# Kernel optimization log

Measured on AMD Instinct MI355X. Metric: run time of the kernel, lower is better.

Reference implementation:

```python
import jax, jax.numpy as jnp
import numpy as np

EMBED_DIM, NUM_HEADS, LOCAL_SIZE = 256, 4, 15
HEAD_DIM = EMBED_DIM // NUM_HEADS
SCALING = float(HEAD_DIM) ** -0.5


def get_overlap_segments(x, window_size):
    # x: (n, t, d) -> (n, t, window_size, d), zero-padded local windows centered at each position
    n, t, d = x.shape
    p = (window_size - 1) // 2
    xp = jnp.pad(x, ((0, 0), (p, p), (0, 0)))
    idx = jnp.arange(t)[:, None] + jnp.arange(window_size)[None, :]  # (t, w)
    return xp[:, idx]


def setup_inputs():
    key = jax.random.key(0)
    ks = jax.random.split(key, 4)
    B, W, F = 4, 64, 4096
    T = W + F
    x = jax.random.normal(ks[0], (B, T, EMBED_DIM), dtype=jnp.float32)
    # block one-hot frame->window assignment (each window owns F//W consecutive frames)
    assign = jnp.repeat(jnp.arange(W), F // W)
    wm = jnp.broadcast_to(jax.nn.one_hot(assign, W, dtype=jnp.float32).T[None], (B, W, F))
    W_qkv = jax.random.normal(ks[1], (EMBED_DIM, 3 * EMBED_DIM), jnp.float32) * 0.02
    b_qkv = jnp.zeros((3 * EMBED_DIM,), jnp.float32)
    W_out = jax.random.normal(ks[2], (EMBED_DIM, EMBED_DIM), jnp.float32) * 0.02
    b_out = jnp.zeros((EMBED_DIM,), jnp.float32)
    return {"x": x, "window_mapping": wm, "W_qkv": W_qkv, "b_qkv": b_qkv,
            "W_out": W_out, "b_out": b_out}


def _to_heads(z, b, t):
    # (b, t, E) -> (b*H, t, d), matching torch transpose/reshape ordering (b outer, h inner)
    return z.reshape(b, t, NUM_HEADS, HEAD_DIM).transpose(0, 2, 1, 3).reshape(b * NUM_HEADS, t, HEAD_DIM)


def reference(x, window_mapping, W_qkv, b_qkv, W_out, b_out):
    b, t, e = x.shape
    Wn, Fn = window_mapping.shape[1], window_mapping.shape[2]
    qkv = x @ W_qkv + b_qkv
    Q, K, V = jnp.split(qkv, 3, axis=-1)
    Q = Q * SCALING
    wtok = _to_heads(x[:, :Wn], b, Wn)            # (n, W, d) raw word tokens
    Qh = _to_heads(Q, b, t)[:, Wn:]               # (n, F, d)
    Kh = _to_heads(K, b, t)[:, Wn:]
    Vh = _to_heads(V, b, t)[:, Wn:]
    wm = jnp.broadcast_to(window_mapping[:, None], (b, NUM_HEADS, Wn, Fn)).reshape(b * NUM_HEADS, Wn, Fn)
    # scatter each window's word token to its frames
    expa = jnp.einsum('nwd,nwf->nfd', wtok, wm)   # (n, F, d)
    Kseg = get_overlap_segments(Kh, LOCAL_SIZE)   # (n, F, w, d)
    Vseg = get_overlap_segments(Vh, LOCAL_SIZE)
    Kcat = jnp.concatenate([expa[:, :, None], Kseg], axis=2)  # (n, F, 1+w, d)
    scores = jnp.einsum('nfd,nfwd->nfw', Qh, Kcat)            # (n, F, 1+w)
    # word-token weight: softmax across frames within each window chunk (F % W == 0, no pad)
    chunk = Fn // Wn
    w_wtok = jax.nn.softmax(scores[:, :, 0].reshape(-1, Wn, chunk), axis=-1).reshape(-1, Fn)
    # local-window weights: softmax over the window axis
    w_fea = jax.nn.softmax(scores[:, :, 1:], axis=-1)
    attn = jnp.concatenate([w_wtok[:, :, None], w_fea], axis=2)  # (n, F, 1+w)
    Vcat = jnp.concatenate([expa[:, :, None], Vseg], axis=2)
    out_fea = jnp.einsum('nfw,nfwd->nfd', attn, Vcat)            # (n, F, d)
    out = jnp.concatenate([wtok, out_fea], axis=1)               # (n, T, d)
    out = out.reshape(b, NUM_HEADS, t, HEAD_DIM).transpose(0, 2, 1, 3).reshape(b, t, e)
    return out @ W_out + b_out
```

## Files before the change

### kernel.cpp

```cpp
#include <hip/hip_runtime.h>


#define QN 4194304ull

typedef _Float16 h8 __attribute__((ext_vector_type(8)));
typedef _Float16 h4 __attribute__((ext_vector_type(4)));
typedef _Float16 h2 __attribute__((ext_vector_type(2)));
typedef float f32x16 __attribute__((ext_vector_type(16)));

__global__ __launch_bounds__(256) void conv_small(
    const float* __restrict__ x,
    const float* __restrict__ Wq, const float* __restrict__ Wo,
    _Float16* __restrict__ wqth, _Float16* __restrict__ woth,
    _Float16* __restrict__ xh) {
  const int g = blockIdx.x, tid = threadIdx.x;
  if (g < 768) {
    int o = g * 256 + tid;
    int n = o >> 8, k = o & 255;
    wqth[o] = (_Float16)Wq[(size_t)k * 768 + n];
  } else if (g < 1024) {
    int o = (g - 768) * 256 + tid;
    int n = o >> 8, k = o & 255;
    woth[o] = (_Float16)Wo[(size_t)k * 256 + n];
  } else {
    size_t base = (size_t)(g - 1024) * 4096 + (size_t)tid * 4;
#pragma unroll
    for (int c = 0; c < 4; ++c) {
      float4 v = *(const float4*)(x + base + c * 1024);
      h4 hv = {(_Float16)v.x, (_Float16)v.y, (_Float16)v.z, (_Float16)v.w};
      *(h4*)(xh + base + c * 1024) = hv;
    }
  }
}

__global__ __launch_bounds__(256) void qkv_mfma(
    const _Float16* __restrict__ xh, const _Float16* __restrict__ wth,
    const float* __restrict__ bq,
    _Float16* __restrict__ Qh, _Float16* __restrict__ Kh,
    _Float16* __restrict__ Vh) {
  __shared__ _Float16 Ah[128][40], Bh[128][40];
  const int tid = threadIdx.x;
  const int wave = tid >> 6, lane = tid & 63;
  const int ln = lane & 31, half = lane >> 5;
  const int mw = (wave & 1) * 64, nw = (wave >> 1) * 64;
  const int m0 = blockIdx.x * 128, n0 = blockIdx.y * 128;

  const int sr = tid >> 1, scq = (tid & 1) * 16;
  const int am = m0 + sr;
  const size_t arow =
      ((size_t)((am >> 12) * 4160 + 64 + (am & 4095))) * 256 + scq;
  const size_t brow = (size_t)(n0 + sr) * 256 + scq;

  float4 rah0, rah1, rbh0, rbh1;
  auto QLOAD = [&](int k0_) {
    rah0 = *(const float4*)(xh + arow + k0_);
    rah1 = *(const float4*)(xh + arow + k0_ + 8);
    rbh0 = *(const float4*)(wth + brow + k0_);
    rbh1 = *(const float4*)(wth + brow + k0_ + 8);
  };

  QLOAD(0);
  f32x16 acc[2][2] = {};

  for (int it = 0; it < 8; ++it) {
    __syncthreads();
    *(float4*)&Ah[sr][scq] = rah0;
    *(float4*)&Ah[sr][scq + 8] = rah1;
    *(float4*)&Bh[sr][scq] = rbh0;
    *(float4*)&Bh[sr][scq + 8] = rbh1;
    __syncthreads();
    if (it < 7) QLOAD((it + 1) * 32);
#pragma unroll
    for (int ks = 0; ks < 2; ++ks) {
      const int kc = ks * 16 + half * 8;
      h8 a0 = *(const h8*)&Ah[mw + ln][kc];
      h8 a1 = *(const h8*)&Ah[mw + 32 + ln][kc];
      h8 b0 = *(const h8*)&Bh[nw + ln][kc];
      h8 b1 = *(const h8*)&Bh[nw + 32 + ln][kc];
      acc[0][0] = __builtin_amdgcn_mfma_f32_32x32x16_f16(a0, b0, acc[0][0], 0, 0, 0);
      acc[0][1] = __builtin_amdgcn_mfma_f32_32x32x16_f16(a0, b1, acc[0][1], 0, 0, 0);
      acc[1][0] = __builtin_amdgcn_mfma_f32_32x32x16_f16(a1, b0, acc[1][0], 0, 0, 0);
      acc[1][1] = __builtin_amdgcn_mfma_f32_32x32x16_f16(a1, b1, acc[1][1], 0, 0, 0);
    }
  }

#pragma unroll
  for (int ni = 0; ni < 2; ++ni) {
    const int c = n0 + nw + ni * 32 + ln;
    const int which = c >> 8, e = c & 255;
    const int h = e >> 6, d = e & 63;
    _Float16* dst = (which == 0) ? Qh : (which == 1) ? Kh : Vh;
    const float sc2 = (which == 0) ? 0.125f : 1.0f;
    const float bias = bq[c];
#pragma unroll
    for (int mi = 0; mi < 2; ++mi) {
      const int rb = m0 + mw + mi * 32 + 4 * half;
#pragma unroll
      for (int reg = 0; reg < 16; ++reg) {
        int rr = rb + (reg & 3) + 8 * (reg >> 2);
        int b2 = rr >> 12, f2 = rr & 4095;
        dst[(((size_t)(b2 * 4 + h)) * 4096 + f2) * 64 + d] =
            (_Float16)((acc[mi][ni][reg] + bias) * sc2);
      }
    }
  }
}

__global__ __launch_bounds__(256) void attn_fused(
    const _Float16* __restrict__ Qh, const _Float16* __restrict__ Kh,
    const _Float16* __restrict__ Vh, const _Float16* __restrict__ xh,
    _Float16* __restrict__ OFh) {
  __shared__ _Float16 Ks[78][72];
  __shared__ _Float16 Vs[78][72];
  __shared__ float s0s[64];
  __shared__ float red[2];
  const int tid = threadIdx.x;
  const int w = blockIdx.x;
  const int n = blockIdx.y;
  const int f0 = w * 64;
  const int b = n >> 2, h = n & 3;

  for (int idx = tid; idx < 78 * 8; idx += 256) {
    int rr = idx >> 3, c = (idx & 7) * 8;
    int g = f0 - 7 + rr;
    h8 k8 = {}, v8 = {};
    if (g >= 0 && g < 4096) {
      size_t base = ((size_t)n * 4096 + g) * 64 + c;
      k8 = *(const h8*)(Kh + base);
      v8 = *(const h8*)(Vh + base);
    }
    *(h8*)&Ks[rr][c] = k8;
    *(h8*)&Vs[rr][c] = v8;
  }
  __syncthreads();

  const int i = tid >> 2, q = tid & 3;
  const size_t qbase = ((size_t)n * 4096 + f0 + i) * 64 + q * 16;
  h8 qh0 = *(const h8*)(Qh + qbase);
  h8 qh1 = *(const h8*)(Qh + qbase + 8);
  const size_t wbase = ((size_t)(b * 4160 + w)) * 256 + h * 64 + q * 16;
  h8 e0 = *(const h8*)(xh + wbase);
  h8 e1 = *(const h8*)(xh + wbase + 8);

  auto dot8 = [](h8 a, h8 bb, float s) {
    s = __builtin_amdgcn_fdot2((h2){a.s0, a.s1}, (h2){bb.s0, bb.s1}, s, false);
    s = __builtin_amdgcn_fdot2((h2){a.s2, a.s3}, (h2){bb.s2, bb.s3}, s, false);
    s = __builtin_amdgcn_fdot2((h2){a.s4, a.s5}, (h2){bb.s4, bb.s5}, s, false);
    s = __builtin_amdgcn_fdot2((h2){a.s6, a.s7}, (h2){bb.s6, bb.s7}, s, false);
    return s;
  };

  float s0 = dot8(qh1, e1, dot8(qh0, e0, 0.f));
  s0 += __shfl_xor(s0, 1);
  s0 += __shfl_xor(s0, 2);

  float sj[15];
#pragma unroll
  for (int j = 0; j < 15; ++j) {
    h8 k0 = *(const h8*)&Ks[i + j][q * 16];
    h8 k1 = *(const h8*)&Ks[i + j][q * 16 + 8];
    float s = dot8(qh1, k1, dot8(qh0, k0, 0.f));
    s += __shfl_xor(s, 1);
    s += __shfl_xor(s, 2);
    sj[j] = s;
  }

  if (q == 0) s0s[i] = s0;
  __syncthreads();
  if (tid < 64) {
    float v = s0s[tid];
    float m = v;
    for (int o = 1; o < 64; o <<= 1) m = fmaxf(m, __shfl_xor(m, o));
    float ee = __expf(v - m);
    float s = ee;
    for (int o = 1; o < 64; o <<= 1) s += __shfl_xor(s, o);
    if (tid == 0) { red[0] = m; red[1] = s; }
  }
  __syncthreads();
  const float wt = __expf(s0 - red[0]) / red[1];

  float mx = sj[0];
#pragma unroll
  for (int j = 1; j < 15; ++j) mx = fmaxf(mx, sj[j]);
  float pj[15], den = 0.f;
#pragma unroll
  for (int j = 0; j < 15; ++j) { pj[j] = __expf(sj[j] - mx); den += pj[j]; }
  const float inv = 1.0f / den;

  float o[16];
#pragma unroll
  for (int k = 0; k < 8; ++k) o[k] = wt * (float)e0[k];
#pragma unroll
  for (int k = 0; k < 8; ++k) o[8 + k] = wt * (float)e1[k];
#pragma unroll
  for (int j = 0; j < 15; ++j) {
    float wj = pj[j] * inv;
    h8 v0 = *(const h8*)&Vs[i + j][q * 16];
    h8 v1 = *(const h8*)&Vs[i + j][q * 16 + 8];
    o[0] = fmaf(wj, (float)v0.s0, o[0]);
    o[1] = fmaf(wj, (float)v0.s1, o[1]);
    o[2] = fmaf(wj, (float)v0.s2, o[2]);
    o[3] = fmaf(wj, (float)v0.s3, o[3]);
    o[4] = fmaf(wj, (float)v0.s4, o[4]);
    o[5] = fmaf(wj, (float)v0.s5, o[5]);
    o[6] = fmaf(wj, (float)v0.s6, o[6]);
    o[7] = fmaf(wj, (float)v0.s7, o[7]);
    o[8] = fmaf(wj, (float)v1.s0, o[8]);
    o[9] = fmaf(wj, (float)v1.s1, o[9]);
    o[10] = fmaf(wj, (float)v1.s2, o[10]);
    o[11] = fmaf(wj, (float)v1.s3, o[11]);
    o[12] = fmaf(wj, (float)v1.s4, o[12]);
    o[13] = fmaf(wj, (float)v1.s5, o[13]);
    o[14] = fmaf(wj, (float)v1.s6, o[14]);
    o[15] = fmaf(wj, (float)v1.s7, o[15]);
  }
  _Float16 oh[16];
#pragma unroll
  for (int dd = 0; dd < 16; ++dd) oh[dd] = (_Float16)o[dd];
  *(float4*)(OFh + qbase) = *(float4*)&oh[0];
  *(float4*)(OFh + qbase + 8) = *(float4*)&oh[8];
}

__global__ __launch_bounds__(256) void out_mfma(
    const _Float16* __restrict__ xh, const _Float16* __restrict__ ofh,
    const _Float16* __restrict__ wth, const float* __restrict__ bo,
    float* __restrict__ out) {
  __shared__ _Float16 Ah[64][72], Bh[128][72];
  const int tid = threadIdx.x;
  const int wave = tid >> 6, lane = tid & 63;
  const int ln = lane & 31, half = lane >> 5;
  const int mw = (wave & 1) * 32, nw = (wave >> 1) * 64;
  const int m0 = blockIdx.x * 64, n0 = blockIdx.y * 128;

  const int sr = tid >> 2, sc4 = (tid & 3) * 16;
  const int sr2 = tid >> 1, sc2 = (tid & 1) * 32;

  const int m = m0 + sr;
  const int b = m / 4160, tt = m % 4160;
  const bool useX = (tt < 64);
  const size_t xrow = ((size_t)(b * 4160 + tt)) * 256 + sc4;
  const long obase = ((long)(b * 4) * 4096 + (tt - 64)) * 64 + sc4;
  const size_t bbase = (size_t)(n0 + sr2) * 256 + sc2;

  float4 ra0, ra1, rb0, rb1, rb2, rb3;
  auto OLOAD = [&](int k0_) {
    if (useX) {
      ra0 = *(const float4*)(xh + xrow + k0_);
      ra1 = *(const float4*)(xh + xrow + k0_ + 8);
    } else {
      size_t o_ = (size_t)(obase + (long)(k0_ >> 6) * 262144);
      ra0 = *(const float4*)(ofh + o_);
      ra1 = *(const float4*)(ofh + o_ + 8);
    }
    rb0 = *(const float4*)(wth + bbase + k0_);
    rb1 = *(const float4*)(wth + bbase + k0_ + 8);
    rb2 = *(const float4*)(wth + bbase + k0_ + 16);
    rb3 = *(const float4*)(wth + bbase + k0_ + 24);
  };

  OLOAD(0);
  f32x16 acc0 = {}, acc1 = {};
  for (int it = 0; it < 4; ++it) {
    __syncthreads();
    *(float4*)&Ah[sr][sc4] = ra0;
    *(float4*)&Ah[sr][sc4 + 8] = ra1;
    *(float4*)&Bh[sr2][sc2] = rb0;
    *(float4*)&Bh[sr2][sc2 + 8] = rb1;
    *(float4*)&Bh[sr2][sc2 + 16] = rb2;
    *(float4*)&Bh[sr2][sc2 + 24] = rb3;
    __syncthreads();
    if (it < 3) OLOAD((it + 1) * 64);
#pragma unroll
    for (int ks = 0; ks < 4; ++ks) {
      const int kc = ks * 16 + half * 8;
      h8 ah = *(const h8*)&Ah[mw + ln][kc];
      h8 b0 = *(const h8*)&Bh[nw + ln][kc];
      h8 b1 = *(const h8*)&Bh[nw + 32 + ln][kc];
      acc0 = __builtin_amdgcn_mfma_f32_32x32x16_f16(ah, b0, acc0, 0, 0, 0);
      acc1 = __builtin_amdgcn_mfma_f32_32x32x16_f16(ah, b1, acc1, 0, 0, 0);
    }
  }
  const int rb = m0 + mw + 4 * half;
#pragma unroll
  for (int ni = 0; ni < 2; ++ni) {
    const int c = n0 + nw + ni * 32 + ln;
    const float bias = bo[c];
    const f32x16& a = ni ? acc1 : acc0;
#pragma unroll
    for (int reg = 0; reg < 16; ++reg) {
      int rr = rb + (reg & 3) + 8 * (reg >> 2);
      out[(size_t)rr * 256 + c] = a[reg] + bias;
    }
  }
}

extern "C" void kernel_launch(void* const* d_in, const int* in_sizes, int n_in,
                              void* d_out, int out_size, void* d_ws, size_t ws_size,
                              hipStream_t stream) {
  const float* x  = (const float*)d_in[0];
  const float* Wq = (const float*)d_in[2];
  const float* bq = (const float*)d_in[3];
  const float* Wo = (const float*)d_in[4];
  const float* bo = (const float*)d_in[5];
  float* out = (float*)d_out;

  _Float16* Qh   = (_Float16*)d_ws;
  _Float16* Kh   = Qh + QN;
  _Float16* Vh   = Kh + QN;
  _Float16* OFh  = Vh + QN;
  _Float16* Wqth = OFh + QN;
  _Float16* Woth = Wqth + 196608;
  _Float16* xh   = Woth + 65536;

  conv_small<<<dim3(2064), 256, 0, stream>>>(x, Wq, Wo, Wqth, Woth, xh);
  qkv_mfma<<<dim3(128, 6), 256, 0, stream>>>(xh, Wqth, bq, Qh, Kh, Vh);
  attn_fused<<<dim3(64, 16), 256, 0, stream>>>(Qh, Kh, Vh, xh, OFh);
  out_mfma<<<dim3(260, 2), 256, 0, stream>>>(xh, OFh, Woth, bo, out);
}
```

Measured before the change: 115.4 us.

## Fuse x fp16 conversion into QKV GEMM and shrink pre-conversion kernel

The QKV GEMM now reads fp32 x directly and converts to fp16 in registers, so the full-x conversion pass is gone. Only the 64 word-token rows per batch are still converted to fp16 (needed later by attention and the output GEMM), along with the W_out transpose. Both are done by an extra row of blocks in the GEMM grid. The W_qkv transpose moves to a small kernel that uses LDS tiling for coalesced reads and writes. The trade-off is that the GEMM reads twice the bytes for its A operand.

```diff
diff --git a/kernel.cpp b/kernel.cpp
--- a/kernel.cpp
+++ b/kernel.cpp
@@ -8,38 +8,77 @@
 typedef _Float16 h2 __attribute__((ext_vector_type(2)));
 typedef float f32x16 __attribute__((ext_vector_type(16)));
 
-__global__ __launch_bounds__(256) void conv_small(
-    const float* __restrict__ x,
-    const float* __restrict__ Wq, const float* __restrict__ Wo,
-    _Float16* __restrict__ wqth, _Float16* __restrict__ woth,
-    _Float16* __restrict__ xh) {
-  const int g = blockIdx.x, tid = threadIdx.x;
-  if (g < 768) {
-    int o = g * 256 + tid;
-    int n = o >> 8, k = o & 255;
-    wqth[o] = (_Float16)Wq[(size_t)k * 768 + n];
-  } else if (g < 1024) {
-    int o = (g - 768) * 256 + tid;
-    int n = o >> 8, k = o & 255;
-    woth[o] = (_Float16)Wo[(size_t)k * 256 + n];
-  } else {
-    size_t base = (size_t)(g - 1024) * 4096 + (size_t)tid * 4;
-#pragma unroll
-    for (int c = 0; c < 4; ++c) {
-      float4 v = *(const float4*)(x + base + c * 1024);
-      h4 hv = {(_Float16)v.x, (_Float16)v.y, (_Float16)v.z, (_Float16)v.w};
-      *(h4*)(xh + base + c * 1024) = hv;
-    }
+__global__ __launch_bounds__(256) void wq_t(
+    const float* __restrict__ Wq, _Float16* __restrict__ wqth) {
+  __shared__ float S[64 * 65];
+  const int id = blockIdx.x, tid = threadIdx.x;
+  const int k0 = (id & 3) * 64, n0 = (id >> 2) * 64;
+  {
+    const int r = tid >> 2, c0 = (tid & 3) * 16;
+    const float* src = Wq + (size_t)(k0 + r) * 768 + n0 + c0;
+#pragma unroll
+    for (int cc = 0; cc < 16; cc += 4)
+      *(float4*)&S[r * 65 + c0 + cc] = *(const float4*)(src + cc);
+  }
+  __syncthreads();
+  {
+    const int nl = tid >> 2, kl0 = (tid & 3) * 16;
+    _Float16 hh[16];
+#pragma unroll
+    for (int j = 0; j < 16; ++j) hh[j] = (_Float16)S[(kl0 + j) * 65 + nl];
+    size_t o = (size_t)(n0 + nl) * 256 + k0 + kl0;
+    *(float4*)(wqth + o) = *(float4*)&hh[0];
+    *(float4*)(wqth + o + 8) = *(float4*)&hh[8];
   }
 }
 
 __global__ __launch_bounds__(256) void qkv_mfma(
-    const _Float16* __restrict__ xh, const _Float16* __restrict__ wth,
+    const float* __restrict__ x, const _Float16* __restrict__ wth,
     const float* __restrict__ bq,
     _Float16* __restrict__ Qh, _Float16* __restrict__ Kh,
-    _Float16* __restrict__ Vh) {
-  __shared__ _Float16 Ah[128][40], Bh[128][40];
+    _Float16* __restrict__ Vh,
+    const float* __restrict__ Wo, _Float16* __restrict__ woth,
+    _Float16* __restrict__ xh) {
+  __shared__ __align__(16) char LDSA[20480];
   const int tid = threadIdx.x;
+
+  if (blockIdx.y == 6) {
+    const int u = blockIdx.x;
+    if (u < 16) {
+      float* S = (float*)LDSA;
+      const int k0 = (u & 3) * 64, n0 = (u >> 2) * 64;
+      {
+        const int r = tid >> 2, c0 = (tid & 3) * 16;
+        const float* src = Wo + (size_t)(k0 + r) * 256 + n0 + c0;
+#pragma unroll
+        for (int cc = 0; cc < 16; cc += 4)
+          *(float4*)&S[r * 65 + c0 + cc] = *(const float4*)(src + cc);
+      }
+      __syncthreads();
+      {
+        const int nl = tid >> 2, kl0 = (tid & 3) * 16;
+        _Float16 hh[16];
+#pragma unroll
+        for (int j = 0; j < 16; ++j) hh[j] = (_Float16)S[(kl0 + j) * 65 + nl];
+        size_t o = (size_t)(n0 + nl) * 256 + k0 + kl0;
+        *(float4*)(woth + o) = *(float4*)&hh[0];
+        *(float4*)(woth + o + 8) = *(float4*)&hh[8];
+      }
+    } else if (u < 20) {
+      const size_t base = (size_t)(u - 16) * 4160 * 256;
+#pragma unroll
+      for (int c = 0; c < 16; ++c) {
+        size_t off = base + (size_t)tid * 4 + (size_t)c * 1024;
+        float4 v = *(const float4*)(x + off);
+        h4 hv = {(_Float16)v.x, (_Float16)v.y, (_Float16)v.z, (_Float16)v.w};
+        *(h4*)(xh + off) = hv;
+      }
+    }
+    return;
+  }
+
+  _Float16(*Ah)[40] = (_Float16(*)[40])LDSA;
+  _Float16(*Bh)[40] = (_Float16(*)[40])(LDSA + 10240);
   const int wave = tid >> 6, lane = tid & 63;
   const int ln = lane & 31, half = lane >> 5;
   const int mw = (wave & 1) * 64, nw = (wave >> 1) * 64;
@@ -53,10 +92,19 @@
 
   float4 rah0, rah1, rbh0, rbh1;
   auto QLOAD = [&](int k0_) {
-    rah0 = *(const float4*)(xh + arow + k0_);
-    rah1 = *(const float4*)(xh + arow + k0_ + 8);
+    float4 fx0 = *(const float4*)(x + arow + k0_);
+    float4 fx1 = *(const float4*)(x + arow + k0_ + 4);
+    float4 fx2 = *(const float4*)(x + arow + k0_ + 8);
+    float4 fx3 = *(const float4*)(x + arow + k0_ + 12);
     rbh0 = *(const float4*)(wth + brow + k0_);
     rbh1 = *(const float4*)(wth + brow + k0_ + 8);
+    _Float16 hh[16] = {
+        (_Float16)fx0.x, (_Float16)fx0.y, (_Float16)fx0.z, (_Float16)fx0.w,
+        (_Float16)fx1.x, (_Float16)fx1.y, (_Float16)fx1.z, (_Float16)fx1.w,
+        (_Float16)fx2.x, (_Float16)fx2.y, (_Float16)fx2.z, (_Float16)fx2.w,
+        (_Float16)fx3.x, (_Float16)fx3.y, (_Float16)fx3.z, (_Float16)fx3.w};
+    rah0 = *(float4*)&hh[0];
+    rah1 = *(float4*)&hh[8];
   };
 
   QLOAD(0);
@@ -312,8 +360,9 @@
   _Float16* Woth = Wqth + 196608;
   _Float16* xh   = Woth + 65536;
 
-  conv_small<<<dim3(2064), 256, 0, stream>>>(x, Wq, Wo, Wqth, Woth, xh);
-  qkv_mfma<<<dim3(128, 6), 256, 0, stream>>>(xh, Wqth, bq, Qh, Kh, Vh);
+  wq_t<<<dim3(48), 256, 0, stream>>>(Wq, Wqth);
+  qkv_mfma<<<dim3(128, 7), 256, 0, stream>>>(x, Wqth, bq, Qh, Kh, Vh, Wo,
+                                             Woth, xh);
   attn_fused<<<dim3(64, 16), 256, 0, stream>>>(Qh, Kh, Vh, xh, OFh);
   out_mfma<<<dim3(260, 2), 256, 0, stream>>>(xh, OFh, Woth, bo, out);
 }
```

Measured after the change: 114.7 us. About the same (-0.6%).
